# Kernel optimization log

Measured on AMD Instinct MI355X. Metric: run time of the kernel, lower is better.

The kernel has to match this reference:

```python
import jax, jax.numpy as jnp
import numpy as np

# Module hyperparameters (init_kwargs): d_in=256, d_out=512, nh=8 -> dv=dk=dd=64
D_IN, D_OUT, NH = 256, 512, 8
DV = D_OUT // NH   # 64
DK = DV            # 64
DD = DK            # 64
KH, KW = 3, 7
D_HID = NH * DK + DK + DV  # 640 (kernel_type='VplusR')
EPS = 1e-6


def l2norm(x, axis):
    # matches torch: x / sqrt(sum(x^2) + eps)
    return x / jnp.sqrt(jnp.sum(x * x, axis=axis, keepdims=True) + EPS)


def conv_same(x, w, groups=1):
    # x: NHWC, w: HWIO, 'same' padding matching torch pad=(KH//2, KW//2)
    return jax.lax.conv_general_dilated(
        x, w, window_strides=(1, 1),
        padding=((KH // 2, KH // 2), (KW // 2, KW // 2)),
        dimension_numbers=('NHWC', 'HWIO', 'NHWC'),
        feature_group_count=groups)


def setup_inputs() -> dict:
    key = jax.random.key(0)
    ks = jax.random.split(key, 8)
    x = jax.random.normal(ks[0], (8, 64, 32, D_IN), jnp.float32)  # [N, T, H, C]
    # projection_linear: two bias-free Linears (torch weight [out, in])
    W1 = jax.random.normal(ks[1], (D_HID, D_IN), jnp.float32) / np.sqrt(D_IN)
    W2 = jax.random.normal(ks[2], (D_HID, D_HID), jnp.float32) / np.sqrt(D_HID)
    # P1 init: randn(dk, dd) * sqrt(1/(ksize*dd))
    P1 = jax.random.normal(ks[3], (DK, DD), jnp.float32) * np.sqrt(1.0 / (KH * KW * DD))
    # H1: grouped Conv2d(dk, dk*dd, groups=dk) -> HWIO weight (KH, KW, 1, DK*DD)
    H1_w = jax.random.normal(ks[4], (KH, KW, 1, DK * DD), jnp.float32) / np.sqrt(KH * KW)
    # H2: Conv2d(1, dd) -> (KH, KW, 1, DD)
    H2_w = jax.random.normal(ks[5], (KH, KW, 1, DD), jnp.float32) / np.sqrt(KH * KW)
    # G: Conv2d(1, dv) -> (KH, KW, 1, DV)
    G_w = jax.random.normal(ks[6], (KH, KW, 1, DV), jnp.float32) / np.sqrt(KH * KW)
    I = jnp.eye(DK, dtype=jnp.float32)  # self.I parameter (identity init)
    return {"x": x, "W1": W1, "W2": W2, "P1": P1,
            "H1_w": H1_w, "H2_w": H2_w, "G_w": G_w, "I": I}


def reference(x, W1, W2, P1, H1_w, H2_w, G_w, I):
    b, T, H, _ = x.shape
    # projection_linear: Linear -> SiLU -> Linear on channel dim
    xp = jax.nn.silu(x @ W1.T) @ W2.T                      # [b,T,H,d_hid]
    q = xp[..., : NH * DK].reshape(b, T, H, NH, DK)        # 'b t h (nh k)'
    k = xp[..., NH * DK : NH * DK + DK]                    # [b,T,H,DK]
    v = xp[..., NH * DK + DK :]                            # [b,T,H,DV]
    q = l2norm(q, axis=-1)
    k = l2norm(k, axis=-1)
    v = l2norm(v, axis=-1)
    # H1: grouped depthwise-style conv generating per-pixel dk x dd kernels
    K_H1 = conv_same(k, H1_w, groups=DK).reshape(b, T, H, DK, DD) + P1
    # kernel = einsum over dk: [b,T,H,NH,DD]
    kernel = jnp.einsum('bthnk,bthkd->bthnd', q, K_H1)
    # H2 / G applied independently to each of the DV channels of v (shared weights):
    # torch treats (b v) as batch with 1 channel; equivalent grouped conv with tiled weight.
    V = conv_same(v, jnp.tile(H2_w, (1, 1, 1, DV)), groups=DV).reshape(b, T, H, DV, DD)
    V_G = conv_same(v, jnp.tile(G_w, (1, 1, 1, DV)), groups=DV).reshape(b, T, H, DV, DV) + I
    # feature = einsum('abc,abd->acd', V_G, V): contract over first dv index
    feature = jnp.einsum('bthvc,bthvd->bthcd', V_G, V)     # [b,T,H,DV,DD]
    # out = einsum('abc,adc->adb', kernel, feature): [bth, DV, NH]
    out = jnp.einsum('bthnd,bthvd->bthvn', kernel, feature)
    # rearrange '(b t h) nh v -> b (nh v) t h' then permute back -> [b,T,H,DV*NH]
    return out.reshape(b, T, H, DV * NH)
```

## Files before the change

### kernel.cpp

```cpp
#include <hip/hip_runtime.h>
#include <hip/hip_bf16.h>

#define NPIX 16384

using short8 = __attribute__((ext_vector_type(8))) short;
using half8  = __attribute__((ext_vector_type(8))) _Float16;
using half4  = __attribute__((ext_vector_type(4))) _Float16;
using half2v = __attribute__((ext_vector_type(2))) _Float16;
using f32x4  = __attribute__((ext_vector_type(4))) float;

__device__ inline short bf16s(float x) {
  __hip_bfloat16 b = __float2bfloat16(x);
  return *reinterpret_cast<short*>(&b);
}

__device__ inline float dot2(half2v a, half2v b, float c) {
#if __has_builtin(__builtin_amdgcn_fdot2)
  return __builtin_amdgcn_fdot2(a, b, c, false);
#else
  return c + (float)a[0] * (float)b[0] + (float)a[1] * (float)b[1];
#endif
}

__global__ __launch_bounds__(256) void cast_bf16(const float* __restrict__ in,
                                                 __hip_bfloat16* __restrict__ out, int n) {
  int i = blockIdx.x * 256 + threadIdx.x;
  int stride = gridDim.x * 256;
  for (; i < n; i += stride) out[i] = __float2bfloat16(in[i]);
}

template<int K>
__global__ __launch_bounds__(256) void gemm_st(const float* __restrict__ Af,
                                               const short* __restrict__ B,
                                               __hip_bfloat16* __restrict__ Cb) {
  __shared__ short As[2][128][36];
  __shared__ short Bs[2][128][36];
  const int tid = threadIdx.x, lane = tid & 63, wid = tid >> 6;
  const int row0 = blockIdx.y * 128, col0 = blockIdx.x * 128;
  const int sr = tid >> 1, sc = (tid & 1) * 16;
  const int l15 = lane & 15, lk = (lane >> 4) * 8;
  const int wr = (wid >> 1) * 64, wc = (wid & 1) * 64;
  const int NS = K / 32;

  short8 aL, aH, bL, bH;
  auto loadTile = [&](int s) {
    const float* src = Af + (size_t)(row0 + sr) * K + s * 32 + sc;
    float4 f0 = *(const float4*)(src);
    float4 f1 = *(const float4*)(src + 4);
    float4 f2 = *(const float4*)(src + 8);
    float4 f3 = *(const float4*)(src + 12);
    aL[0] = bf16s(f0.x); aL[1] = bf16s(f0.y); aL[2] = bf16s(f0.z); aL[3] = bf16s(f0.w);
    aL[4] = bf16s(f1.x); aL[5] = bf16s(f1.y); aL[6] = bf16s(f1.z); aL[7] = bf16s(f1.w);
    aH[0] = bf16s(f2.x); aH[1] = bf16s(f2.y); aH[2] = bf16s(f2.z); aH[3] = bf16s(f2.w);
    aH[4] = bf16s(f3.x); aH[5] = bf16s(f3.y); aH[6] = bf16s(f3.z); aH[7] = bf16s(f3.w);
    const short* srcB = B + (size_t)(col0 + sr) * K + s * 32 + sc;
    bL = *(const short8*)srcB;
    bH = *(const short8*)(srcB + 8);
  };
  auto writeTile = [&](int buf) {
    *(short8*)&As[buf][sr][sc]     = aL;
    *(short8*)&As[buf][sr][sc + 8] = aH;
    *(short8*)&Bs[buf][sr][sc]     = bL;
    *(short8*)&Bs[buf][sr][sc + 8] = bH;
  };

  loadTile(0);
  writeTile(0);
  __syncthreads();

  f32x4 acc[4][4];
#pragma unroll
  for (int mi = 0; mi < 4; ++mi)
#pragma unroll
    for (int nj = 0; nj < 4; ++nj) acc[mi][nj] = (f32x4){0.f, 0.f, 0.f, 0.f};

  for (int s = 0; s < NS; ++s) {
    const int cur = s & 1;
    if (s + 1 < NS) loadTile(s + 1);
    short8 af[4], bfr[4];
#pragma unroll
    for (int mi = 0; mi < 4; ++mi)
      af[mi] = *(const short8*)&As[cur][wr + mi * 16 + l15][lk];
#pragma unroll
    for (int nj = 0; nj < 4; ++nj)
      bfr[nj] = *(const short8*)&Bs[cur][wc + nj * 16 + l15][lk];
#pragma unroll
    for (int mi = 0; mi < 4; ++mi)
#pragma unroll
      for (int nj = 0; nj < 4; ++nj)
        acc[mi][nj] = __builtin_amdgcn_mfma_f32_16x16x32_bf16(af[mi], bfr[nj], acc[mi][nj], 0, 0, 0);
    if (s + 1 < NS) writeTile(cur ^ 1);
    __syncthreads();
  }

  const int r0 = (lane >> 4) * 4;
#pragma unroll
  for (int mi = 0; mi < 4; ++mi)
#pragma unroll
    for (int nj = 0; nj < 4; ++nj)
#pragma unroll
      for (int r = 0; r < 4; ++r) {
        int row = row0 + wr + mi * 16 + r0 + r;
        int col = col0 + wc + nj * 16 + l15;
        float v = acc[mi][nj][r];
        v = v / (1.f + __expf(-v));
        Cb[(size_t)row * 640 + col] = __float2bfloat16(v);
      }
}

__global__ __launch_bounds__(256) void gemm_qkv(const short* __restrict__ Ab,
                                                const short* __restrict__ B,
                                                _Float16* __restrict__ qn,
                                                _Float16* __restrict__ kn,
                                                _Float16* __restrict__ vn) {
  __shared__ short As[2][128][36];
  __shared__ short Bs[2][128][36];
  const int tid = threadIdx.x, lane = tid & 63, wid = tid >> 6;
  const int row0 = blockIdx.y * 128, col0 = blockIdx.x * 128;
  const int sr = tid >> 1, sc = (tid & 1) * 16;
  const int l15 = lane & 15, lk = (lane >> 4) * 8;
  const int wr = (wid >> 1) * 64, wc = (wid & 1) * 64;
  const int NS = 20;

  short8 aL, aH, bL, bH;
  auto loadTile = [&](int s) {
    const short* src = Ab + (size_t)(row0 + sr) * 640 + s * 32 + sc;
    aL = *(const short8*)src;
    aH = *(const short8*)(src + 8);
    const short* srcB = B + (size_t)(col0 + sr) * 640 + s * 32 + sc;
    bL = *(const short8*)srcB;
    bH = *(const short8*)(srcB + 8);
  };
  auto writeTile = [&](int buf) {
    *(short8*)&As[buf][sr][sc]     = aL;
    *(short8*)&As[buf][sr][sc + 8] = aH;
    *(short8*)&Bs[buf][sr][sc]     = bL;
    *(short8*)&Bs[buf][sr][sc + 8] = bH;
  };

  loadTile(0);
  writeTile(0);
  __syncthreads();

  f32x4 acc[4][4];
#pragma unroll
  for (int mi = 0; mi < 4; ++mi)
#pragma unroll
    for (int nj = 0; nj < 4; ++nj) acc[mi][nj] = (f32x4){0.f, 0.f, 0.f, 0.f};

  for (int s = 0; s < NS; ++s) {
    const int cur = s & 1;
    if (s + 1 < NS) loadTile(s + 1);
    short8 af[4], bfr[4];
#pragma unroll
    for (int mi = 0; mi < 4; ++mi)
      af[mi] = *(const short8*)&As[cur][wr + mi * 16 + l15][lk];
#pragma unroll
    for (int nj = 0; nj < 4; ++nj)
      bfr[nj] = *(const short8*)&Bs[cur][wc + nj * 16 + l15][lk];
#pragma unroll
    for (int mi = 0; mi < 4; ++mi)
#pragma unroll
      for (int nj = 0; nj < 4; ++nj)
        acc[mi][nj] = __builtin_amdgcn_mfma_f32_16x16x32_bf16(af[mi], bfr[nj], acc[mi][nj], 0, 0, 0);
    if (s + 1 < NS) writeTile(cur ^ 1);
    __syncthreads();
  }

  const int r0g = (lane >> 4) * 4;
  const int ct = blockIdx.x;
  const int colh = wid & 1;
#pragma unroll
  for (int mi = 0; mi < 4; ++mi)
#pragma unroll
    for (int r = 0; r < 4; ++r) {
      float s = 0.f;
#pragma unroll
      for (int nj = 0; nj < 4; ++nj) s += acc[mi][nj][r] * acc[mi][nj][r];
      s += __shfl_xor(s, 1); s += __shfl_xor(s, 2);
      s += __shfl_xor(s, 4); s += __shfl_xor(s, 8);
      float inv = 1.f / sqrtf(s + 1e-6f);
      int row = row0 + wr + mi * 16 + r0g + r;
      _Float16* dst;
      if (ct < 4) dst = qn + (size_t)row * 512 + (ct * 2 + colh) * 64;
      else        dst = (colh == 0 ? kn : vn) + (size_t)row * 64;
#pragma unroll
      for (int nj = 0; nj < 4; ++nj)
        dst[nj * 16 + l15] = (_Float16)(acc[mi][nj][r] * inv);
    }
}

__global__ __launch_bounds__(256) void wt_build(const float* __restrict__ H1w,
                                                const float* __restrict__ P1,
                                                const float* __restrict__ H2w,
                                                _Float16* __restrict__ Wt,
                                                _Float16* __restrict__ H2h) {
  int i = blockIdx.x * 256 + threadIdx.x;
  if (i < 64 * 1408) {
    int d = i & 63, k = i >> 6;
    float v;
    if (k < 1344) { int t = k >> 6, c = k & 63; v = H1w[t * 4096 + c * 64 + d]; }
    else          { int c = k - 1344;          v = P1[c * 64 + d]; }
    Wt[(size_t)d * 1408 + k] = (_Float16)v;
  } else if (i < 64 * 1408 + 2048) {
    int j = i - 64 * 1408;
    int t = j >> 6, d = j & 63;
    H2h[j] = (t < 21) ? (_Float16)H2w[t * 64 + d] : (_Float16)0.f;
  }
}

__global__ __launch_bounds__(256, 4) void fused_kp(const _Float16* __restrict__ qn_g,
                                                   const _Float16* __restrict__ kn,
                                                   const _Float16* __restrict__ vn,
                                                   const _Float16* __restrict__ Wt,
                                                   const _Float16* __restrict__ H2h,
                                                   const float* __restrict__ Gw,
                                                   float* __restrict__ out) {
  __shared__ _Float16 qn_s[128][72];
  __shared__ _Float16 win[66][72];
  __shared__ _Float16 Bt[2][64][40];

  float*    Zs  = (float*)&qn_s[0][0];
  _Float16* ZMs = (_Float16*)((char*)&qn_s[0][0] + 10752);
  _Float16* Gt  = &Bt[0][0][0];
  _Float16* GwS = &Bt[0][0][0] + 2576;

  int tid = threadIdx.x, lane = tid & 63, wid = tid >> 6;
  int pb = blockIdx.x * 16;
  int h0 = pb & 31, t0 = (pb >> 5) & 63, batch = pb >> 11;
  const int sd = tid >> 2, skq = (tid & 3) * 8;
  const int rt0 = wid * 2;
  const int l15 = lane & 15, lk = (lane >> 4) * 8;

  half8 q00, q01, q10, q11;
  int pix0, pix1;
  {
    int grow0 = (rt0 + 0) * 16 + l15;
    int grow1 = (rt0 + 1) * 16 + l15;
    pix0 = grow0 >> 3; pix1 = grow1 >> 3;
    const _Float16* b = qn_g + (size_t)pb * 512;
    q00 = *(const half8*)(b + grow0 * 64 + lk);
    q01 = *(const half8*)(b + grow0 * 64 + 32 + lk);
    q10 = *(const half8*)(b + grow1 * 64 + lk);
    q11 = *(const half8*)(b + grow1 * 64 + 32 + lk);
  }

  for (int idx = tid; idx < 528; idx += 256) {
    int j = idx >> 3, c0 = (idx & 7) * 8;
    int dy = j / 22, hx = j % 22;
    int t = t0 - 1 + dy, h = h0 - 3 + hx;
    half8 v = {0, 0, 0, 0, 0, 0, 0, 0};
    if ((unsigned)t < 64u && (unsigned)h < 32u)
      v = *(const half8*)(kn + ((size_t)((batch * 64 + t) * 32 + h)) * 64 + c0);
    *(half8*)&win[j][c0] = v;
  }
  *(half8*)&Bt[0][sd][skq] = *(const half8*)(Wt + (size_t)sd * 1408 + skq);
  __syncthreads();

  f32x4 acc[2][4];
#pragma unroll
  for (int rt = 0; rt < 2; ++rt)
#pragma unroll
    for (int nj = 0; nj < 4; ++nj) acc[rt][nj] = (f32x4){0.f, 0.f, 0.f, 0.f};

  for (int ss = 0; ss < 22; ++ss) {
    const int sA = ss * 2, sB = sA + 1;
    const int dy = ss / 7, dxx = ss % 7;

    {
      half8 stage = *(const half8*)(Wt + (size_t)sd * 1408 + (sA + 1) * 32 + skq);
      half8 bfr[4];
#pragma unroll
      for (int nj = 0; nj < 4; ++nj)
        bfr[nj] = *(const half8*)&Bt[0][nj * 16 + l15][lk];
      half8 a0, a1;
      if (ss < 21) {
        a0 = q00 * *(const half8*)&win[dy * 22 + pix0 + dxx][lk];
        a1 = q10 * *(const half8*)&win[dy * 22 + pix1 + dxx][lk];
      } else {
        a0 = q00; a1 = q10;
      }
#pragma unroll
      for (int nj = 0; nj < 4; ++nj) {
        acc[0][nj] = __builtin_amdgcn_mfma_f32_16x16x32_f16(a0, bfr[nj], acc[0][nj], 0, 0, 0);
        acc[1][nj] = __builtin_amdgcn_mfma_f32_16x16x32_f16(a1, bfr[nj], acc[1][nj], 0, 0, 0);
      }
      *(half8*)&Bt[1][sd][skq] = stage;
      __syncthreads();
    }
    {
      half8 stage;
      if (sB < 43)
        stage = *(const half8*)(Wt + (size_t)sd * 1408 + (sB + 1) * 32 + skq);
      half8 bfr[4];
#pragma unroll
      for (int nj = 0; nj < 4; ++nj)
        bfr[nj] = *(const half8*)&Bt[1][nj * 16 + l15][lk];
      half8 a0, a1;
      if (ss < 21) {
        a0 = q01 * *(const half8*)&win[dy * 22 + pix0 + dxx][32 + lk];
        a1 = q11 * *(const half8*)&win[dy * 22 + pix1 + dxx][32 + lk];
      } else {
        a0 = q01; a1 = q11;
      }
#pragma unroll
      for (int nj = 0; nj < 4; ++nj) {
        acc[0][nj] = __builtin_amdgcn_mfma_f32_16x16x32_f16(a0, bfr[nj], acc[0][nj], 0, 0, 0);
        acc[1][nj] = __builtin_amdgcn_mfma_f32_16x16x32_f16(a1, bfr[nj], acc[1][nj], 0, 0, 0);
      }
      if (sB < 43) *(half8*)&Bt[0][sd][skq] = stage;
      __syncthreads();
    }
  }

  _Float16* kld = &qn_s[0][0];
  const int r0 = (lane >> 4) * 4;
#pragma unroll
  for (int rt = 0; rt < 2; ++rt) {
    int growb = (rt0 + rt) * 16;
#pragma unroll
    for (int nj = 0; nj < 4; ++nj)
#pragma unroll
      for (int r = 0; r < 4; ++r)
        kld[(growb + r0 + r) * 72 + nj * 16 + l15] = (_Float16)acc[rt][nj][r];
  }

  f32x4 accZ[2][2];
#pragma unroll
  for (int rt = 0; rt < 2; ++rt)
#pragma unroll
    for (int ct = 0; ct < 2; ++ct) accZ[rt][ct] = (f32x4){0.f, 0.f, 0.f, 0.f};
#pragma unroll
  for (int k2 = 0; k2 < 2; ++k2) {
    half8 bz[2];
#pragma unroll
    for (int ct = 0; ct < 2; ++ct)
      bz[ct] = *(const half8*)(H2h + (ct * 16 + l15) * 64 + k2 * 32 + lk);
#pragma unroll
    for (int rt = 0; rt < 2; ++rt) {
      half8 az = *(const half8*)&kld[((rt0 + rt) * 16 + l15) * 72 + k2 * 32 + lk];
#pragma unroll
      for (int ct = 0; ct < 2; ++ct)
        accZ[rt][ct] = __builtin_amdgcn_mfma_f32_16x16x32_f16(az, bz[ct], accZ[rt][ct], 0, 0, 0);
    }
  }
  __syncthreads();

#pragma unroll
  for (int rt = 0; rt < 2; ++rt)
#pragma unroll
    for (int ct = 0; ct < 2; ++ct) {
      int t = ct * 16 + l15;
      if (t < 21) {
#pragma unroll
        for (int r = 0; r < 4; ++r) {
          int grow = (rt0 + rt) * 16 + r0 + r;
          Zs[((grow >> 3) * 21 + t) * 8 + (grow & 7)] = accZ[rt][ct][r];
        }
      }
    }
  for (int idx = tid; idx < 528; idx += 256) {
    int j = idx >> 3, c0 = (idx & 7) * 8;
    int dy = j / 22, hx = j % 22;
    int t = t0 - 1 + dy, h = h0 - 3 + hx;
    half8 v = {0, 0, 0, 0, 0, 0, 0, 0};
    if ((unsigned)t < 64u && (unsigned)h < 32u)
      v = *(const half8*)(vn + ((size_t)((batch * 64 + t) * 32 + h)) * 64 + c0);
    *(half8*)&win[j][c0] = v;
  }
  for (int idx = tid; idx < 168; idx += 256) {
    int t = idx >> 3, c0 = (idx & 7) * 8;
    const float* g = Gw + t * 64 + c0;
    half8 o;
#pragma unroll
    for (int j = 0; j < 8; ++j) o[j] = (_Float16)g[j];
    *(half8*)&GwS[t * 64 + c0] = o;
  }
  __syncthreads();

  for (int task = tid; task < 2574; task += 256) {
    int g = task / 286, rem = task % 286;
    int x1 = rem / 13, d = rem % 13;
    int x2 = x1 + d - 6;
    float s = 0.f;
    if ((unsigned)x2 < 22u) {
      const _Float16* a = &win[(g / 3) * 22 + x1][0];
      const _Float16* b = &win[(g % 3) * 22 + x2][0];
#pragma unroll
      for (int c8 = 0; c8 < 8; ++c8) {
        half8 av = *(const half8*)(a + c8 * 8);
        half8 bv = *(const half8*)(b + c8 * 8);
        s = dot2((half2v){av[0], av[1]}, (half2v){bv[0], bv[1]}, s);
        s = dot2((half2v){av[2], av[3]}, (half2v){bv[2], bv[3]}, s);
        s = dot2((half2v){av[4], av[5]}, (half2v){bv[4], bv[5]}, s);
        s = dot2((half2v){av[6], av[7]}, (half2v){bv[6], bv[7]}, s);
      }
    }
    Gt[task] = (_Float16)s;
  }
  __syncthreads();

  for (int task = tid; task < 336; task += 256) {
    int pix = task / 21, t1 = task % 21;
    int dy1 = t1 / 7, dx1i = t1 % 7;
    int x1 = pix + dx1i;
    f32x4 s0 = {0.f, 0.f, 0.f, 0.f}, s1 = {0.f, 0.f, 0.f, 0.f};
#pragma unroll
    for (int t2 = 0; t2 < 21; ++t2) {
      float m = (float)Gt[(dy1 * 3 + t2 / 7) * 286 + x1 * 13 + (t2 % 7) - dx1i + 6];
      s0 += m * *(const f32x4*)&Zs[(pix * 21 + t2) * 8];
      s1 += m * *(const f32x4*)&Zs[(pix * 21 + t2) * 8 + 4];
    }
    half4 lo = {(_Float16)s0[0], (_Float16)s0[1], (_Float16)s0[2], (_Float16)s0[3]};
    half4 hi = {(_Float16)s1[0], (_Float16)s1[1], (_Float16)s1[2], (_Float16)s1[3]};
    *(half4*)&ZMs[(pix * 21 + t1) * 8]     = lo;
    *(half4*)&ZMs[(pix * 21 + t1) * 8 + 4] = hi;
  }
  __syncthreads();

  for (int task = tid; task < 512; task += 256) {
    int pix = task >> 5, v0 = (task & 31) * 2;
    f32x4 a0[2] = {{0.f,0.f,0.f,0.f},{0.f,0.f,0.f,0.f}};
    f32x4 a1[2] = {{0.f,0.f,0.f,0.f},{0.f,0.f,0.f,0.f}};
#pragma unroll
    for (int t = 0; t < 21; ++t) {
      half2v sv = *(const half2v*)&win[(t / 7) * 22 + pix + (t % 7)][v0];
      half2v gw = *(const half2v*)&GwS[t * 64 + v0];
      f32x4 z0 = *(const f32x4*)&Zs[(pix * 21 + t) * 8];
      f32x4 z1 = *(const f32x4*)&Zs[(pix * 21 + t) * 8 + 4];
      half8 zm = *(const half8*)&ZMs[(pix * 21 + t) * 8];
      f32x4 m0 = {(float)zm[0], (float)zm[1], (float)zm[2], (float)zm[3]};
      f32x4 m1 = {(float)zm[4], (float)zm[5], (float)zm[6], (float)zm[7]};
#pragma unroll
      for (int j = 0; j < 2; ++j) {
        float svf = (float)sv[j], gwf = (float)gw[j];
        a0[j] += svf * z0 + gwf * m0;
        a1[j] += svf * z1 + gwf * m1;
      }
    }
#pragma unroll
    for (int j = 0; j < 2; ++j) {
      float* dst = out + (size_t)(pb + pix) * 512 + (v0 + j) * 8;
      *(f32x4*)dst = a0[j];
      *(f32x4*)(dst + 4) = a1[j];
    }
  }
}

extern "C" void kernel_launch(void* const* d_in, const int* in_sizes, int n_in,
                              void* d_out, int out_size, void* d_ws, size_t ws_size,
                              hipStream_t stream) {
  const float* x   = (const float*)d_in[0];
  const float* W1  = (const float*)d_in[1];
  const float* W2  = (const float*)d_in[2];
  const float* P1  = (const float*)d_in[3];
  const float* H1w = (const float*)d_in[4];
  const float* H2w = (const float*)d_in[5];
  const float* Gw  = (const float*)d_in[6];
  float* out = (float*)d_out;

  char* ws = (char*)d_ws;
  __hip_bfloat16* h_bf = (__hip_bfloat16*)(ws);
  _Float16* qn         = (_Float16*)(ws + 20971520);
  _Float16* kn         = (_Float16*)(ws + 37748736);
  _Float16* vn         = (_Float16*)(ws + 39845888);
  __hip_bfloat16* W1_bf= (__hip_bfloat16*)(ws + 41943040);
  __hip_bfloat16* W2_bf= (__hip_bfloat16*)(ws + 42270720);
  _Float16* Wt         = (_Float16*)(ws + 43089920);
  _Float16* H2h        = (_Float16*)(ws + 43270144);

  cast_bf16<<<dim3(160), dim3(256), 0, stream>>>(W1, W1_bf, 640 * 256);
  cast_bf16<<<dim3(400), dim3(256), 0, stream>>>(W2, W2_bf, 640 * 640);

  gemm_st<256><<<dim3(5, 128), dim3(256), 0, stream>>>(x, (const short*)W1_bf, h_bf);
  gemm_qkv<<<dim3(5, 128), dim3(256), 0, stream>>>(
      (const short*)h_bf, (const short*)W2_bf, qn, kn, vn);

  wt_build<<<dim3(361), dim3(256), 0, stream>>>(H1w, P1, H2w, Wt, H2h);

  fused_kp<<<dim3(NPIX / 16), dim3(256), 0, stream>>>(qn, kn, vn, Wt, H2h, Gw, out);
}
```

Before: 127.0 us.

## Compute window Gram matrix with MFMA and merge weight-prep kernels

Replaces the scalar fdot2 loop that builds the pairwise window inner products (Gt) with 16x16x32 f16 MFMA tiles, computing only upper-triangular tiles and writing mirrored entries by symmetry. Also folds the two weight-cast launches and the Wt/H2h build into a single prep kernel to cut launch overhead. Invalid Gt slots are no longer zeroed, relying on the consumer never reading them.

```diff
diff --git a/kernel.cpp b/kernel.cpp
--- a/kernel.cpp
+++ b/kernel.cpp
@@ -14,19 +14,33 @@
   return *reinterpret_cast<short*>(&b);
 }
 
-__device__ inline float dot2(half2v a, half2v b, float c) {
-#if __has_builtin(__builtin_amdgcn_fdot2)
-  return __builtin_amdgcn_fdot2(a, b, c, false);
-#else
-  return c + (float)a[0] * (float)b[0] + (float)a[1] * (float)b[1];
-#endif
-}
-
-__global__ __launch_bounds__(256) void cast_bf16(const float* __restrict__ in,
-                                                 __hip_bfloat16* __restrict__ out, int n) {
+__global__ __launch_bounds__(256) void prep_all(const float* __restrict__ W1,
+                                                const float* __restrict__ W2,
+                                                const float* __restrict__ H1w,
+                                                const float* __restrict__ P1,
+                                                const float* __restrict__ H2w,
+                                                __hip_bfloat16* __restrict__ W1_bf,
+                                                __hip_bfloat16* __restrict__ W2_bf,
+                                                _Float16* __restrict__ Wt,
+                                                _Float16* __restrict__ H2h) {
   int i = blockIdx.x * 256 + threadIdx.x;
-  int stride = gridDim.x * 256;
-  for (; i < n; i += stride) out[i] = __float2bfloat16(in[i]);
+  const int n1 = 640 * 256, n2 = 640 * 640, n3 = 64 * 1408;
+  if (i < n1) {
+    W1_bf[i] = __float2bfloat16(W1[i]);
+  } else if (i < n1 + n2) {
+    W2_bf[i - n1] = __float2bfloat16(W2[i - n1]);
+  } else if (i < n1 + n2 + n3) {
+    int j = i - n1 - n2;
+    int dd = j & 63, k = j >> 6;
+    float v;
+    if (k < 1344) { int t = k >> 6, c = k & 63; v = H1w[t * 4096 + c * 64 + dd]; }
+    else          { int c = k - 1344;          v = P1[c * 64 + dd]; }
+    Wt[(size_t)dd * 1408 + k] = (_Float16)v;
+  } else if (i < n1 + n2 + n3 + 2048) {
+    int j = i - n1 - n2 - n3;
+    int t = j >> 6, dd = j & 63;
+    H2h[j] = (t < 21) ? (_Float16)H2w[t * 64 + dd] : (_Float16)0.f;
+  }
 }
 
 template<int K>
@@ -190,25 +204,6 @@
     }
 }
 
-__global__ __launch_bounds__(256) void wt_build(const float* __restrict__ H1w,
-                                                const float* __restrict__ P1,
-                                                const float* __restrict__ H2w,
-                                                _Float16* __restrict__ Wt,
-                                                _Float16* __restrict__ H2h) {
-  int i = blockIdx.x * 256 + threadIdx.x;
-  if (i < 64 * 1408) {
-    int d = i & 63, k = i >> 6;
-    float v;
-    if (k < 1344) { int t = k >> 6, c = k & 63; v = H1w[t * 4096 + c * 64 + d]; }
-    else          { int c = k - 1344;          v = P1[c * 64 + d]; }
-    Wt[(size_t)d * 1408 + k] = (_Float16)v;
-  } else if (i < 64 * 1408 + 2048) {
-    int j = i - 64 * 1408;
-    int t = j >> 6, d = j & 63;
-    H2h[j] = (t < 21) ? (_Float16)H2w[t * 64 + d] : (_Float16)0.f;
-  }
-}
-
 __global__ __launch_bounds__(256, 4) void fused_kp(const _Float16* __restrict__ qn_g,
                                                    const _Float16* __restrict__ kn,
                                                    const _Float16* __restrict__ vn,
@@ -378,25 +373,41 @@
   }
   __syncthreads();
 
-  for (int task = tid; task < 2574; task += 256) {
-    int g = task / 286, rem = task % 286;
-    int x1 = rem / 13, d = rem % 13;
-    int x2 = x1 + d - 6;
-    float s = 0.f;
-    if ((unsigned)x2 < 22u) {
-      const _Float16* a = &win[(g / 3) * 22 + x1][0];
-      const _Float16* b = &win[(g % 3) * 22 + x2][0];
-#pragma unroll
-      for (int c8 = 0; c8 < 8; ++c8) {
-        half8 av = *(const half8*)(a + c8 * 8);
-        half8 bv = *(const half8*)(b + c8 * 8);
-        s = dot2((half2v){av[0], av[1]}, (half2v){bv[0], bv[1]}, s);
-        s = dot2((half2v){av[2], av[3]}, (half2v){bv[2], bv[3]}, s);
-        s = dot2((half2v){av[4], av[5]}, (half2v){bv[4], bv[5]}, s);
-        s = dot2((half2v){av[6], av[7]}, (half2v){bv[6], bv[7]}, s);
-      }
-    }
-    Gt[task] = (_Float16)s;
+  {
+    const half8 hz = {0, 0, 0, 0, 0, 0, 0, 0};
+    int c = 0;
+#pragma unroll
+    for (int ti = 0; ti < 5; ++ti)
+#pragma unroll
+      for (int tj = ti; tj < 5; ++tj, ++c) {
+        if ((c & 3) == wid) {
+          f32x4 g = {0.f, 0.f, 0.f, 0.f};
+          const int ra = ti * 16 + l15, rb = tj * 16 + l15;
+#pragma unroll
+          for (int k2 = 0; k2 < 2; ++k2) {
+            half8 av = (ra < 66) ? *(const half8*)&win[ra][k2 * 32 + lk] : hz;
+            half8 bv = (rb < 66) ? *(const half8*)&win[rb][k2 * 32 + lk] : hz;
+            g = __builtin_amdgcn_mfma_f32_16x16x32_f16(av, bv, g, 0, 0, 0);
+          }
+#pragma unroll
+          for (int r = 0; r < 4; ++r) {
+            int j1 = ti * 16 + r0 + r, j2 = tj * 16 + l15;
+            if (j1 < 66 && j2 < 66) {
+              int dy1 = j1 / 22, x1 = j1 % 22;
+              int dy2 = j2 / 22, x2 = j2 % 22;
+              int d = x2 - x1 + 6;
+              _Float16 val = (_Float16)g[r];
+              if ((unsigned)d < 13u)
+                Gt[(dy1 * 3 + dy2) * 286 + x1 * 13 + d] = val;
+              if (ti != tj) {
+                int d2 = 12 - d;
+                if ((unsigned)d2 < 13u)
+                  Gt[(dy2 * 3 + dy1) * 286 + x2 * 13 + d2] = val;
+              }
+            }
+          }
+        }
+      }
   }
   __syncthreads();
 
@@ -469,14 +480,12 @@
   _Float16* Wt         = (_Float16*)(ws + 43089920);
   _Float16* H2h        = (_Float16*)(ws + 43270144);
 
-  cast_bf16<<<dim3(160), dim3(256), 0, stream>>>(W1, W1_bf, 640 * 256);
-  cast_bf16<<<dim3(400), dim3(256), 0, stream>>>(W2, W2_bf, 640 * 640);
+  prep_all<<<dim3(2600), dim3(256), 0, stream>>>(W1, W2, H1w, P1, H2w,
+                                                 W1_bf, W2_bf, Wt, H2h);
 
   gemm_st<256><<<dim3(5, 128), dim3(256), 0, stream>>>(x, (const short*)W1_bf, h_bf);
   gemm_qkv<<<dim3(5, 128), dim3(256), 0, stream>>>(
       (const short*)h_bf, (const short*)W2_bf, qn, kn, vn);
 
-  wt_build<<<dim3(361), dim3(256), 0, stream>>>(H1w, P1, H2w, Wt, H2h);
-
   fused_kp<<<dim3(NPIX / 16), dim3(256), 0, stream>>>(qn, kn, vn, Wt, H2h, Gw, out);
 }
```

Result: faster. 119.7 us (-5.8%).
